# Kernel optimization log

Measured on AMD Instinct MI355X. Metric: run time of the kernel, lower is better.

Reference implementation:

```python
import jax, jax.numpy as jnp
import numpy as np

N = 50000        # num nodes
E = 800000       # num edges (avg degree 16)
IN_DIM = 64
OUT_DIM = 64
PE_DIM = 24
HEADS = 2
HID = OUT_DIM * HEADS  # 128


def setup_inputs() -> dict:
    key = jax.random.key(0)
    ks = jax.random.split(key, 16)
    std = 0.1  # trunc_normal_(std=0.1) init in the torch module
    return {
        "x": jax.random.normal(ks[0], (N, IN_DIM), jnp.float32),
        "pe_index": jax.random.randint(ks[1], (2, E), 0, N, jnp.int32),
        "pe_val": jax.random.normal(ks[2], (E, PE_DIM), jnp.float32),
        # edge-weight MLP (blocks): input proj, one residual FFN block, final proj
        "W_in": jax.random.normal(ks[3], (PE_DIM, HID), jnp.float32) * std,
        "b_in": jnp.zeros((HID,), jnp.float32),
        "W1": jax.random.normal(ks[4], (HID, HID), jnp.float32) * std,
        "b1": jnp.zeros((HID,), jnp.float32),
        "W2": jax.random.normal(ks[5], (HID, HID), jnp.float32) * std,
        "b2": jnp.zeros((HID,), jnp.float32),
        "W_fin": jax.random.normal(ks[6], (HID, HID), jnp.float32) * std,
        "b_fin": jnp.zeros((HID,), jnp.float32),
        # node feature -> multi-head projection
        "W_x": jax.random.normal(ks[7], (IN_DIM, HID), jnp.float32) * std,
        "b_x": jnp.zeros((HID,), jnp.float32),
        # per-head output bias
        "head_bias": jnp.zeros((1, HEADS, OUT_DIM), jnp.float32),
        # final out projection
        "W_out": jax.random.normal(ks[8], (HID, OUT_DIM), jnp.float32) * std,
        "b_out": jnp.zeros((OUT_DIM,), jnp.float32),
    }


def _edge_mlp(pe, W_in, b_in, W1, b1, W2, b2, W_fin, b_fin):
    # Linear(pe_dim->hid), then residual block [GELU, Linear, GELU, Linear, +res], then Linear(hid->hid)
    g = lambda t: jax.nn.gelu(t, approximate=False)  # torch nn.GELU default = exact erf
    x0 = pe @ W_in + b_in                     # [E, HID]
    h = g(x0) @ W1 + b1
    h = g(h) @ W2 + b2
    x0 = h + x0                               # ResidualLayer: x + x_res
    return x0 @ W_fin + b_fin                 # [E, HID]


def reference(x, pe_index, pe_val, W_in, b_in, W1, b1, W2, b2, W_fin, b_fin,
              W_x, b_x, head_bias, W_out, b_out):
    tgt = pe_index[0]  # messages aggregate to edge_index[0]
    src = pe_index[1]
    score = _edge_mlp(pe_val, W_in, b_in, W1, b1, W2, b2, W_fin, b_fin)
    score = score.reshape(-1, HEADS, OUT_DIM)                 # [E, H, D]
    xh = (x @ W_x + b_x).reshape(-1, HEADS, OUT_DIM)          # [N, H, D]
    msg = xh[src] * score                                     # gather-multiply
    wV = jax.ops.segment_sum(msg, tgt, num_segments=N)        # scatter-add [N, H, D]
    deg = jax.ops.segment_sum(jnp.ones((msg.shape[0],), jnp.float32), tgt, num_segments=N)
    wV = wV / jnp.maximum(deg, 1.0)[:, None, None]            # average=True -> mean aggregation
    h = (wV + head_bias).reshape(-1, HEADS * OUT_DIM)
    return h @ W_out + b_out                                  # out_proj: [N, OUT_DIM]
```

## Files before the change

### kernel.cpp

```cpp
#include <hip/hip_runtime.h>
#include <hip/hip_bf16.h>
#include <math.h>

#define NN 50000
#define EE 800000
#define HID 128
#define PED 24
#define IND 64
#define OUTD 64
#define EBLK 128
#define AKS 136

typedef short bf16x8 __attribute__((ext_vector_type(8)));
typedef float f32x4 __attribute__((ext_vector_type(4)));

__device__ __forceinline__ float gelu_fast(float x) {
    float x2 = x * x;
    float t = __builtin_fmaf(x2, -0.07135481627f, -1.5957691216f);
    float e = __expf(x * t);
    return x * __builtin_amdgcn_rcpf(1.0f + e);
}
__device__ __forceinline__ unsigned short f2bf(float f) {
    unsigned int u = __float_as_uint(f);
    u = (u + 0x7fffu + ((u >> 16) & 1u)) >> 16;
    return (unsigned short)u;
}
__device__ __forceinline__ unsigned int pkbf2(float a, float b) {
    __hip_bfloat162 h = __float22bfloat162_rn(make_float2(a, b));
    return *reinterpret_cast<unsigned int*>(&h);
}
__device__ __forceinline__ float bflo(unsigned int u) {
    return __uint_as_float(u << 16);
}
__device__ __forceinline__ float bfhi(unsigned int u) {
    return __uint_as_float(u & 0xffff0000u);
}

__global__ __launch_bounds__(256) void pre_kernel(
    const float* __restrict__ x, const float* __restrict__ W_x,
    const float* __restrict__ b_x, unsigned short* __restrict__ xhb,
    const float* __restrict__ W_in, const float* __restrict__ W1,
    const float* __restrict__ W2, const float* __restrict__ Wf,
    unsigned short* __restrict__ WT_in, unsigned short* __restrict__ WT1,
    unsigned short* __restrict__ WT2, unsigned short* __restrict__ WTf,
    float* __restrict__ wV, int* __restrict__ cnt) {
    int bx = blockIdx.x;
    if (bx < 6250) {
        int gid = bx * 256 + threadIdx.x;
        int n = gid >> 5;
        int q = gid & 31;
        *(float4*)&wV[(size_t)n * HID + q * 4] = make_float4(0.f, 0.f, 0.f, 0.f);
        const float* xr = x + (size_t)n * IND;
        float4 acc = *(const float4*)&b_x[q * 4];
#pragma unroll 8
        for (int k = 0; k < IND; k++) {
            float xk = xr[k];
            float4 w = *(const float4*)&W_x[k * HID + q * 4];
            acc.x += xk * w.x; acc.y += xk * w.y;
            acc.z += xk * w.z; acc.w += xk * w.w;
        }
        uint2 p;
        p.x = pkbf2(acc.x, acc.y);
        p.y = pkbf2(acc.z, acc.w);
        ((uint2*)&xhb[(size_t)n * HID])[q] = p;
    } else {
        int idx = (bx - 6250) * 256 + threadIdx.x;
        if (idx < NN) cnt[idx] = 0;
        if (idx < 4096) {
            int j = idx >> 5, k = idx & 31;
            WT_in[idx] = f2bf(k < PED ? W_in[k * HID + j] : 0.f);
        } else if (idx < 4096 + 16384) {
            int i = idx - 4096; int j = i >> 7, k = i & 127;
            WT1[i] = f2bf(W1[k * HID + j]);
        } else if (idx < 4096 + 32768) {
            int i = idx - 4096 - 16384; int j = i >> 7, k = i & 127;
            WT2[i] = f2bf(W2[k * HID + j]);
        } else if (idx < 4096 + 49152) {
            int i = idx - 4096 - 32768; int j = i >> 7, k = i & 127;
            WTf[i] = f2bf(Wf[k * HID + j]);
        }
    }
}

__global__ __launch_bounds__(256) void hist_kernel(const int* __restrict__ pe_idx,
                                                   int* __restrict__ cnt) {
    int e = blockIdx.x * 256 + threadIdx.x;
    if (e < EE) atomicAdd(&cnt[pe_idx[e]], 1);
}

__global__ __launch_bounds__(1024) void scan_kernel(const int* __restrict__ cnt,
                                                    int* __restrict__ woff) {
    __shared__ int s_w[16];
    int tid = threadIdx.x;
    const int chunk = (NN + 1023) / 1024;
    int base = tid * chunk;
    int end = base + chunk; if (end > NN) end = NN;
    int s = 0;
    for (int i = base; i < end; i++) s += cnt[i];
    int v = s;
    int lane = tid & 63, wid = tid >> 6;
#pragma unroll
    for (int d = 1; d < 64; d <<= 1) {
        int u = __shfl_up(v, d, 64);
        if (lane >= d) v += u;
    }
    if (lane == 63) s_w[wid] = v;
    __syncthreads();
    if (tid < 16) {
        int wv = s_w[tid];
#pragma unroll
        for (int d = 1; d < 16; d <<= 1) {
            int u = __shfl_up(wv, d, 64);
            if (tid >= d) wv += u;
        }
        s_w[tid] = wv;
    }
    __syncthreads();
    int exc = v - s + (wid ? s_w[wid - 1] : 0);
    int run = exc;
    for (int i = base; i < end; i++) { woff[i] = run; run += cnt[i]; }
}

__global__ __launch_bounds__(256) void scatter_kernel(const int* __restrict__ pe_idx,
                                                      int* __restrict__ woff,
                                                      int* __restrict__ perm) {
    int e = blockIdx.x * 256 + threadIdx.x;
    if (e < EE) {
        int t = pe_idx[e];
        int p = atomicAdd(&woff[t], 1);
        perm[p] = e;
    }
}

__global__ __launch_bounds__(512, 4) void edge_kernel(
    const float* __restrict__ pe_val, const int* __restrict__ pe_idx,
    const int* __restrict__ perm, const unsigned short* __restrict__ xhb,
    const unsigned short* __restrict__ WT_in, const unsigned short* __restrict__ WT1,
    const unsigned short* __restrict__ WT2, const unsigned short* __restrict__ WTf,
    const float* __restrict__ b_in, const float* __restrict__ b1,
    const float* __restrict__ b2, const float* __restrict__ bfin,
    float* __restrict__ wV) {
    __shared__ __align__(16) unsigned short s_act[EBLK][AKS];
    __shared__ __align__(16) unsigned short s_W[HID][AKS];
    __shared__ int s_eid[EBLK], s_tgt[EBLK], s_src[EBLK];
    float* s_msg = (float*)&s_W[0][0];

    const int tid = threadIdx.x;
    const int lane = tid & 63;
    const int w = tid >> 6;
    const int cg = w & 3;
    const int eh = w >> 2;
    const int ebase = eh * 64;
    const int l15 = lane & 15;
    const int quad = lane >> 4;
    const long b0 = (long)blockIdx.x * EBLK;

    if (tid < EBLK) {
        int eid = perm[b0 + tid];
        s_eid[tid] = eid;
        s_tgt[tid] = pe_idx[eid];
        s_src[tid] = pe_idx[EE + eid];
    }
#pragma unroll
    for (int i = 0; i < 4; i++) {
        int idx = tid + i * 512; int r = idx >> 4, seg = idx & 15;
        *(uint4*)&s_W[r][seg * 8] = *(const uint4*)&WT1[r * HID + seg * 8];
    }
    __syncthreads();
#pragma unroll
    for (int i = 0; i < 4; i++) {
        int idx = tid + i * 512; int e = idx >> 4, k2 = idx & 15;
        float2 v = make_float2(0.f, 0.f);
        if (k2 < 12) v = *(const float2*)&pe_val[(size_t)s_eid[e] * PED + k2 * 2];
        *(unsigned int*)&s_act[e][k2 * 2] = pkbf2(v.x, v.y);
    }
    __syncthreads();

    f32x4 C[2][4];
    f32x4 x0s[2][4];

    {
        float4 ba = *(const float4*)&b_in[(2 * cg + 0) * 16 + quad * 4];
        float4 bb = *(const float4*)&b_in[(2 * cg + 1) * 16 + quad * 4];
        f32x4 ci0 = {ba.x, ba.y, ba.z, ba.w};
        f32x4 ci1 = {bb.x, bb.y, bb.z, bb.w};
        bf16x8 a0 = *(const bf16x8*)&WT_in[((2 * cg + 0) * 16 + l15) * 32 + quad * 8];
        bf16x8 a1 = *(const bf16x8*)&WT_in[((2 * cg + 1) * 16 + l15) * 32 + quad * 8];
#pragma unroll
        for (int u = 0; u < 4; u++) {
            bf16x8 bfr = *(const bf16x8*)&s_act[ebase + u * 16 + l15][quad * 8];
            C[0][u] = __builtin_amdgcn_mfma_f32_16x16x32_bf16(a0, bfr, ci0, 0, 0, 0);
            C[1][u] = __builtin_amdgcn_mfma_f32_16x16x32_bf16(a1, bfr, ci1, 0, 0, 0);
        }
    }
    __syncthreads();
#pragma unroll
    for (int t = 0; t < 2; t++) {
        int ch0 = (2 * cg + t) * 16 + quad * 4;
#pragma unroll
        for (int u = 0; u < 4; u++) {
            int e = ebase + u * 16 + l15;
            f32x4 c = C[t][u];
            x0s[t][u] = c;
            uint2 p;
            p.x = pkbf2(gelu_fast(c[0]), gelu_fast(c[1]));
            p.y = pkbf2(gelu_fast(c[2]), gelu_fast(c[3]));
            *(uint2*)&s_act[e][ch0] = p;
        }
    }
    __syncthreads();

#define GEMM128(BIAS)                                                          \
    {                                                                          \
        float4 ba_ = *(const float4*)&(BIAS)[(2 * cg + 0) * 16 + quad * 4];    \
        float4 bb_ = *(const float4*)&(BIAS)[(2 * cg + 1) * 16 + quad * 4];    \
        f32x4 ci0 = {ba_.x, ba_.y, ba_.z, ba_.w};                              \
        f32x4 ci1 = {bb_.x, bb_.y, bb_.z, bb_.w};                              \
        _Pragma("unroll") for (int u = 0; u < 4; u++) {                        \
            C[0][u] = ci0; C[1][u] = ci1;                                      \
        }                                                                      \
        _Pragma("unroll") for (int ks = 0; ks < 4; ks++) {                     \
            bf16x8 a0 = *(const bf16x8*)&s_W[(2 * cg + 0) * 16 + l15]          \
                                            [ks * 32 + quad * 8];              \
            bf16x8 a1 = *(const bf16x8*)&s_W[(2 * cg + 1) * 16 + l15]          \
                                            [ks * 32 + quad * 8];              \
            _Pragma("unroll") for (int u = 0; u < 4; u++) {                    \
                bf16x8 bfr = *(const bf16x8*)&s_act[ebase + u * 16 + l15]      \
                                                   [ks * 32 + quad * 8];       \
                C[0][u] = __builtin_amdgcn_mfma_f32_16x16x32_bf16(a0, bfr,     \
                                                                  C[0][u], 0, 0, 0); \
                C[1][u] = __builtin_amdgcn_mfma_f32_16x16x32_bf16(a1, bfr,     \
                                                                  C[1][u], 0, 0, 0); \
            }                                                                  \
        }                                                                      \
    }

#define STAGE_W(WT)                                                            \
    _Pragma("unroll") for (int i = 0; i < 4; i++) {                            \
        int idx = tid + i * 512; int r = idx >> 4, seg = idx & 15;             \
        *(uint4*)&s_W[r][seg * 8] = *(const uint4*)&(WT)[r * HID + seg * 8];   \
    }

    GEMM128(b1);
    __syncthreads();
#pragma unroll
    for (int t = 0; t < 2; t++) {
        int ch0 = (2 * cg + t) * 16 + quad * 4;
#pragma unroll
        for (int u = 0; u < 4; u++) {
            int e = ebase + u * 16 + l15;
            f32x4 c = C[t][u];
            uint2 p;
            p.x = pkbf2(gelu_fast(c[0]), gelu_fast(c[1]));
            p.y = pkbf2(gelu_fast(c[2]), gelu_fast(c[3]));
            *(uint2*)&s_act[e][ch0] = p;
        }
    }
    STAGE_W(WT2);
    __syncthreads();

    GEMM128(b2);
    __syncthreads();
#pragma unroll
    for (int t = 0; t < 2; t++) {
        int ch0 = (2 * cg + t) * 16 + quad * 4;
#pragma unroll
        for (int u = 0; u < 4; u++) {
            int e = ebase + u * 16 + l15;
            f32x4 c = C[t][u];
            f32x4 x0 = x0s[t][u];
            uint2 p;
            p.x = pkbf2(c[0] + x0[0], c[1] + x0[1]);
            p.y = pkbf2(c[2] + x0[2], c[3] + x0[3]);
            *(uint2*)&s_act[e][ch0] = p;
        }
    }
    STAGE_W(WTf);
    __syncthreads();

    GEMM128(bfin);
    uint2 xva[4];
#pragma unroll
    for (int i = 0; i < 4; i++) {
        int idx = tid + i * 512; int e = idx >> 5, c4 = idx & 31;
        xva[i] = ((const uint2*)&xhb[(size_t)s_src[e] * HID])[c4];
    }
    __syncthreads();
#pragma unroll
    for (int t = 0; t < 2; t++) {
        int ch0 = (2 * cg + t) * 16 + quad * 4;
#pragma unroll
        for (int u = 0; u < 4; u++) {
            int e = ebase + u * 16 + l15;
            f32x4 c = C[t][u];
            uint2 p;
            p.x = pkbf2(c[0], c[1]);
            p.y = pkbf2(c[2], c[3]);
            *(uint2*)&s_act[e][ch0] = p;
        }
    }
    __syncthreads();

#pragma unroll
    for (int i = 0; i < 4; i++) {
        int idx = tid + i * 512;
        int e = idx >> 5, c4 = idx & 31;
        uint2 xv = xva[i];
        uint2 sv = *(const uint2*)&s_act[e][c4 * 4];
        float4 m;
        m.x = bflo(xv.x) * bflo(sv.x);
        m.y = bfhi(xv.x) * bfhi(sv.x);
        m.z = bflo(xv.y) * bflo(sv.y);
        m.w = bfhi(xv.y) * bfhi(sv.y);
        *(float4*)&s_msg[e * HID + c4 * 4] = m;
    }
    uint2 xvb[4];
#pragma unroll
    for (int i = 0; i < 4; i++) {
        int idx = tid + (4 + i) * 512; int e = idx >> 5, c4 = idx & 31;
        xvb[i] = ((const uint2*)&xhb[(size_t)s_src[e] * HID])[c4];
    }
    __syncthreads();

    if (tid < 256) {
        const int h = tid >> 7;
        const int c = tid & 127;
        const int e0 = h * 32;
        float acc = 0.f;
        int prev = s_tgt[e0];
        bool firstseg = true;
        for (int e = e0; e < e0 + 32; e++) {
            int tg = s_tgt[e];
            if (tg != prev) {
                if (firstseg) atomicAdd(&wV[(size_t)prev * HID + c], acc);
                else          wV[(size_t)prev * HID + c] = acc;
                firstseg = false;
                acc = 0.f;
                prev = tg;
            }
            acc += s_msg[e * HID + c];
        }
        atomicAdd(&wV[(size_t)prev * HID + c], acc);
    }
    __syncthreads();

#pragma unroll
    for (int i = 0; i < 4; i++) {
        int idx = tid + (4 + i) * 512;
        int e = idx >> 5, c4 = idx & 31;
        uint2 xv = xvb[i];
        uint2 sv = *(const uint2*)&s_act[e][c4 * 4];
        float4 m;
        m.x = bflo(xv.x) * bflo(sv.x);
        m.y = bfhi(xv.x) * bfhi(sv.x);
        m.z = bflo(xv.y) * bflo(sv.y);
        m.w = bfhi(xv.y) * bfhi(sv.y);
        *(float4*)&s_msg[(e - 64) * HID + c4 * 4] = m;
    }
    __syncthreads();

    if (tid < 256) {
        const int h = tid >> 7;
        const int c = tid & 127;
        const int e0 = 64 + h * 32;
        float acc = 0.f;
        int prev = s_tgt[e0];
        bool firstseg = true;
        for (int e = e0; e < e0 + 32; e++) {
            int tg = s_tgt[e];
            if (tg != prev) {
                if (firstseg) atomicAdd(&wV[(size_t)prev * HID + c], acc);
                else          wV[(size_t)prev * HID + c] = acc;
                firstseg = false;
                acc = 0.f;
                prev = tg;
            }
            acc += s_msg[(e - 64) * HID + c];
        }
        atomicAdd(&wV[(size_t)prev * HID + c], acc);
    }
#undef GEMM128
#undef STAGE_W
}

__global__ __launch_bounds__(256) void out_kernel(
    const float* __restrict__ wV, const int* __restrict__ cnt,
    const float* __restrict__ head_bias, const float* __restrict__ W_out,
    const float* __restrict__ b_out, float* __restrict__ out) {
    int gid = blockIdx.x * 256 + threadIdx.x;
    int n = gid >> 4;
    int q = gid & 15;
    if (n >= NN) return;
    float inv = 1.0f / fmaxf((float)cnt[n], 1.0f);
    const float* wr = wV + (size_t)n * HID;
    float4 acc = *(const float4*)&b_out[q * 4];
#pragma unroll 4
    for (int k = 0; k < HID; k++) {
        float hv = wr[k] * inv + head_bias[k];
        float4 wv4 = *(const float4*)&W_out[k * OUTD + q * 4];
        acc.x += hv * wv4.x; acc.y += hv * wv4.y;
        acc.z += hv * wv4.z; acc.w += hv * wv4.w;
    }
    *(float4*)&out[(size_t)n * OUTD + q * 4] = acc;
}

extern "C" void kernel_launch(void* const* d_in, const int* in_sizes, int n_in,
                              void* d_out, int out_size, void* d_ws, size_t ws_size,
                              hipStream_t stream) {
    const float* x      = (const float*)d_in[0];
    const int*   pe_idx = (const int*)d_in[1];
    const float* pe_val = (const float*)d_in[2];
    const float* W_in   = (const float*)d_in[3];
    const float* b_in   = (const float*)d_in[4];
    const float* W1     = (const float*)d_in[5];
    const float* b1     = (const float*)d_in[6];
    const float* W2     = (const float*)d_in[7];
    const float* b2     = (const float*)d_in[8];
    const float* Wf     = (const float*)d_in[9];
    const float* bfin   = (const float*)d_in[10];
    const float* W_x    = (const float*)d_in[11];
    const float* b_x    = (const float*)d_in[12];
    const float* hb     = (const float*)d_in[13];
    const float* W_out  = (const float*)d_in[14];
    const float* b_out  = (const float*)d_in[15];
    float* out = (float*)d_out;

    float* wV   = (float*)d_ws;
    int*   cnt  = (int*)(wV + (size_t)NN * HID);
    int*   woff = cnt + NN;
    int*   perm = woff + NN;
    unsigned short* WT_in = (unsigned short*)(perm + EE);
    unsigned short* WT1   = WT_in + 128 * 32;
    unsigned short* WT2   = WT1 + 128 * 128;
    unsigned short* WTf   = WT2 + 128 * 128;
    unsigned short* xhb   = WTf + 128 * 128;

    pre_kernel<<<6250 + 208, 256, 0, stream>>>(x, W_x, b_x, xhb,
                                               W_in, W1, W2, Wf,
                                               WT_in, WT1, WT2, WTf, wV, cnt);
    hist_kernel<<<(EE + 255) / 256, 256, 0, stream>>>(pe_idx, cnt);
    scan_kernel<<<1, 1024, 0, stream>>>(cnt, woff);
    scatter_kernel<<<(EE + 255) / 256, 256, 0, stream>>>(pe_idx, woff, perm);

    edge_kernel<<<EE / EBLK, 512, 0, stream>>>(pe_val, pe_idx, perm, xhb,
                                               WT_in, WT1, WT2, WTf,
                                               b_in, b1, b2, bfin, wV);

    out_kernel<<<(NN * 16 + 255) / 256, 256, 0, stream>>>(wV, cnt, hb, W_out,
                                                          b_out, out);
}
```

Baseline: 632.5 us.

## Ping-pong activation buffers, read weights from global, fuse gather into segment reduce

Replaces the shared weight tile with a second activation buffer so consecutive MLP layers alternate between two smem buffers. This removes the weight staging copies and about half of the block barriers, and weight fragments are now read straight from global/L2. The message stage no longer materialises fp32 messages in shared memory. All 512 threads gather source features per channel and multiply with the score inside the segmented reduction, which covers all 128 edges in one pass. The trade-off is more global/L2 traffic for the weights and scalar 2-byte gathers instead of vectorised ones.

New measurement: 702.3 us. 11.0% more time.

```diff
diff --git a/kernel.cpp b/kernel.cpp
--- a/kernel.cpp
+++ b/kernel.cpp
@@ -29,11 +29,8 @@
     __hip_bfloat162 h = __float22bfloat162_rn(make_float2(a, b));
     return *reinterpret_cast<unsigned int*>(&h);
 }
-__device__ __forceinline__ float bflo(unsigned int u) {
-    return __uint_as_float(u << 16);
-}
-__device__ __forceinline__ float bfhi(unsigned int u) {
-    return __uint_as_float(u & 0xffff0000u);
+__device__ __forceinline__ float bf2f(unsigned short u) {
+    return __uint_as_float((unsigned int)u << 16);
 }
 
 __global__ __launch_bounds__(256) void pre_kernel(
@@ -140,10 +137,8 @@
     const float* __restrict__ b_in, const float* __restrict__ b1,
     const float* __restrict__ b2, const float* __restrict__ bfin,
     float* __restrict__ wV) {
-    __shared__ __align__(16) unsigned short s_act[EBLK][AKS];
-    __shared__ __align__(16) unsigned short s_W[HID][AKS];
-    __shared__ int s_eid[EBLK], s_tgt[EBLK], s_src[EBLK];
-    float* s_msg = (float*)&s_W[0][0];
+    __shared__ __align__(16) unsigned short s_act[2][EBLK][AKS];
+    __shared__ int s_tgt[EBLK], s_src[EBLK];
 
     const int tid = threadIdx.x;
     const int lane = tid & 63;
@@ -157,22 +152,18 @@
 
     if (tid < EBLK) {
         int eid = perm[b0 + tid];
-        s_eid[tid] = eid;
         s_tgt[tid] = pe_idx[eid];
         s_src[tid] = pe_idx[EE + eid];
     }
-#pragma unroll
-    for (int i = 0; i < 4; i++) {
-        int idx = tid + i * 512; int r = idx >> 4, seg = idx & 15;
-        *(uint4*)&s_W[r][seg * 8] = *(const uint4*)&WT1[r * HID + seg * 8];
-    }
-    __syncthreads();
 #pragma unroll
     for (int i = 0; i < 4; i++) {
         int idx = tid + i * 512; int e = idx >> 4, k2 = idx & 15;
         float2 v = make_float2(0.f, 0.f);
-        if (k2 < 12) v = *(const float2*)&pe_val[(size_t)s_eid[e] * PED + k2 * 2];
-        *(unsigned int*)&s_act[e][k2 * 2] = pkbf2(v.x, v.y);
+        if (k2 < 12) {
+            int eid = perm[b0 + e];
+            v = *(const float2*)&pe_val[(size_t)eid * PED + k2 * 2];
+        }
+        *(unsigned int*)&s_act[0][e][k2 * 2] = pkbf2(v.x, v.y);
     }
     __syncthreads();
 
@@ -188,12 +179,11 @@
         bf16x8 a1 = *(const bf16x8*)&WT_in[((2 * cg + 1) * 16 + l15) * 32 + quad * 8];
 #pragma unroll
         for (int u = 0; u < 4; u++) {
-            bf16x8 bfr = *(const bf16x8*)&s_act[ebase + u * 16 + l15][quad * 8];
+            bf16x8 bfr = *(const bf16x8*)&s_act[0][ebase + u * 16 + l15][quad * 8];
             C[0][u] = __builtin_amdgcn_mfma_f32_16x16x32_bf16(a0, bfr, ci0, 0, 0, 0);
             C[1][u] = __builtin_amdgcn_mfma_f32_16x16x32_bf16(a1, bfr, ci1, 0, 0, 0);
         }
     }
-    __syncthreads();
 #pragma unroll
     for (int t = 0; t < 2; t++) {
         int ch0 = (2 * cg + t) * 16 + quad * 4;
@@ -205,12 +195,12 @@
             uint2 p;
             p.x = pkbf2(gelu_fast(c[0]), gelu_fast(c[1]));
             p.y = pkbf2(gelu_fast(c[2]), gelu_fast(c[3]));
-            *(uint2*)&s_act[e][ch0] = p;
-        }
-    }
-    __syncthreads();
-
-#define GEMM128(BIAS)                                                          \
+            *(uint2*)&s_act[1][e][ch0] = p;
+        }
+    }
+    __syncthreads();
+
+#define GEMM128(WT, BIAS, SB)                                                  \
     {                                                                          \
         float4 ba_ = *(const float4*)&(BIAS)[(2 * cg + 0) * 16 + quad * 4];    \
         float4 bb_ = *(const float4*)&(BIAS)[(2 * cg + 1) * 16 + quad * 4];    \
@@ -220,12 +210,12 @@
             C[0][u] = ci0; C[1][u] = ci1;                                      \
         }                                                                      \
         _Pragma("unroll") for (int ks = 0; ks < 4; ks++) {                     \
-            bf16x8 a0 = *(const bf16x8*)&s_W[(2 * cg + 0) * 16 + l15]          \
-                                            [ks * 32 + quad * 8];              \
-            bf16x8 a1 = *(const bf16x8*)&s_W[(2 * cg + 1) * 16 + l15]          \
-                                            [ks * 32 + quad * 8];              \
+            bf16x8 a0 = *(const bf16x8*)&(WT)[((2 * cg + 0) * 16 + l15) * HID  \
+                                              + ks * 32 + quad * 8];           \
+            bf16x8 a1 = *(const bf16x8*)&(WT)[((2 * cg + 1) * 16 + l15) * HID  \
+                                              + ks * 32 + quad * 8];           \
             _Pragma("unroll") for (int u = 0; u < 4; u++) {                    \
-                bf16x8 bfr = *(const bf16x8*)&s_act[ebase + u * 16 + l15]      \
+                bf16x8 bfr = *(const bf16x8*)&s_act[SB][ebase + u * 16 + l15]  \
                                                    [ks * 32 + quad * 8];       \
                 C[0][u] = __builtin_amdgcn_mfma_f32_16x16x32_bf16(a0, bfr,     \
                                                                   C[0][u], 0, 0, 0); \
@@ -235,14 +225,7 @@
         }                                                                      \
     }
 
-#define STAGE_W(WT)                                                            \
-    _Pragma("unroll") for (int i = 0; i < 4; i++) {                            \
-        int idx = tid + i * 512; int r = idx >> 4, seg = idx & 15;             \
-        *(uint4*)&s_W[r][seg * 8] = *(const uint4*)&(WT)[r * HID + seg * 8];   \
-    }
-
-    GEMM128(b1);
-    __syncthreads();
+    GEMM128(WT1, b1, 1);
 #pragma unroll
     for (int t = 0; t < 2; t++) {
         int ch0 = (2 * cg + t) * 16 + quad * 4;
@@ -253,14 +236,12 @@
             uint2 p;
             p.x = pkbf2(gelu_fast(c[0]), gelu_fast(c[1]));
             p.y = pkbf2(gelu_fast(c[2]), gelu_fast(c[3]));
-            *(uint2*)&s_act[e][ch0] = p;
-        }
-    }
-    STAGE_W(WT2);
-    __syncthreads();
-
-    GEMM128(b2);
-    __syncthreads();
+            *(uint2*)&s_act[0][e][ch0] = p;
+        }
+    }
+    __syncthreads();
+
+    GEMM128(WT2, b2, 0);
 #pragma unroll
     for (int t = 0; t < 2; t++) {
         int ch0 = (2 * cg + t) * 16 + quad * 4;
@@ -272,20 +253,12 @@
             uint2 p;
             p.x = pkbf2(c[0] + x0[0], c[1] + x0[1]);
             p.y = pkbf2(c[2] + x0[2], c[3] + x0[3]);
-            *(uint2*)&s_act[e][ch0] = p;
-        }
-    }
-    STAGE_W(WTf);
-    __syncthreads();
-
-    GEMM128(bfin);
-    uint2 xva[4];
-#pragma unroll
-    for (int i = 0; i < 4; i++) {
-        int idx = tid + i * 512; int e = idx >> 5, c4 = idx & 31;
-        xva[i] = ((const uint2*)&xhb[(size_t)s_src[e] * HID])[c4];
-    }
-    __syncthreads();
+            *(uint2*)&s_act[1][e][ch0] = p;
+        }
+    }
+    __syncthreads();
+
+    GEMM128(WTf, bfin, 1);
 #pragma unroll
     for (int t = 0; t < 2; t++) {
         int ch0 = (2 * cg + t) * 16 + quad * 4;
@@ -296,91 +269,44 @@
             uint2 p;
             p.x = pkbf2(c[0], c[1]);
             p.y = pkbf2(c[2], c[3]);
-            *(uint2*)&s_act[e][ch0] = p;
-        }
-    }
-    __syncthreads();
-
-#pragma unroll
-    for (int i = 0; i < 4; i++) {
-        int idx = tid + i * 512;
-        int e = idx >> 5, c4 = idx & 31;
-        uint2 xv = xva[i];
-        uint2 sv = *(const uint2*)&s_act[e][c4 * 4];
-        float4 m;
-        m.x = bflo(xv.x) * bflo(sv.x);
-        m.y = bfhi(xv.x) * bfhi(sv.x);
-        m.z = bflo(xv.y) * bflo(sv.y);
-        m.w = bfhi(xv.y) * bfhi(sv.y);
-        *(float4*)&s_msg[e * HID + c4 * 4] = m;
-    }
-    uint2 xvb[4];
-#pragma unroll
-    for (int i = 0; i < 4; i++) {
-        int idx = tid + (4 + i) * 512; int e = idx >> 5, c4 = idx & 31;
-        xvb[i] = ((const uint2*)&xhb[(size_t)s_src[e] * HID])[c4];
-    }
-    __syncthreads();
-
-    if (tid < 256) {
-        const int h = tid >> 7;
+            *(uint2*)&s_act[0][e][ch0] = p;
+        }
+    }
+    __syncthreads();
+
+    {
         const int c = tid & 127;
-        const int e0 = h * 32;
+        const int q = tid >> 7;
+        const int e0 = q * 32;
         float acc = 0.f;
         int prev = s_tgt[e0];
         bool firstseg = true;
-        for (int e = e0; e < e0 + 32; e++) {
-            int tg = s_tgt[e];
-            if (tg != prev) {
-                if (firstseg) atomicAdd(&wV[(size_t)prev * HID + c], acc);
-                else          wV[(size_t)prev * HID + c] = acc;
-                firstseg = false;
-                acc = 0.f;
-                prev = tg;
+#pragma unroll
+        for (int b = 0; b < 4; b++) {
+            float xs[8];
+#pragma unroll
+            for (int j = 0; j < 8; j++) {
+                int e = e0 + b * 8 + j;
+                xs[j] = bf2f(xhb[(size_t)s_src[e] * HID + c]);
             }
-            acc += s_msg[e * HID + c];
+#pragma unroll
+            for (int j = 0; j < 8; j++) {
+                int e = e0 + b * 8 + j;
+                int tg = s_tgt[e];
+                if (tg != prev) {
+                    if (firstseg) atomicAdd(&wV[(size_t)prev * HID + c], acc);
+                    else          wV[(size_t)prev * HID + c] = acc;
+                    firstseg = false;
+                    acc = 0.f;
+                    prev = tg;
+                }
+                float sc = bf2f(s_act[0][e][c]);
+                acc += xs[j] * sc;
+            }
         }
         atomicAdd(&wV[(size_t)prev * HID + c], acc);
     }
-    __syncthreads();
-
-#pragma unroll
-    for (int i = 0; i < 4; i++) {
-        int idx = tid + (4 + i) * 512;
-        int e = idx >> 5, c4 = idx & 31;
-        uint2 xv = xvb[i];
-        uint2 sv = *(const uint2*)&s_act[e][c4 * 4];
-        float4 m;
-        m.x = bflo(xv.x) * bflo(sv.x);
-        m.y = bfhi(xv.x) * bfhi(sv.x);
-        m.z = bflo(xv.y) * bflo(sv.y);
-        m.w = bfhi(xv.y) * bfhi(sv.y);
-        *(float4*)&s_msg[(e - 64) * HID + c4 * 4] = m;
-    }
-    __syncthreads();
-
-    if (tid < 256) {
-        const int h = tid >> 7;
-        const int c = tid & 127;
-        const int e0 = 64 + h * 32;
-        float acc = 0.f;
-        int prev = s_tgt[e0];
-        bool firstseg = true;
-        for (int e = e0; e < e0 + 32; e++) {
-            int tg = s_tgt[e];
-            if (tg != prev) {
-                if (firstseg) atomicAdd(&wV[(size_t)prev * HID + c], acc);
-                else          wV[(size_t)prev * HID + c] = acc;
-                firstseg = false;
-                acc = 0.f;
-                prev = tg;
-            }
-            acc += s_msg[(e - 64) * HID + c];
-        }
-        atomicAdd(&wV[(size_t)prev * HID + c], acc);
-    }
 #undef GEMM128
-#undef STAGE_W
 }
 
 __global__ __launch_bounds__(256) void out_kernel(
```
